# Performance work log

Hardware: AMD Instinct MI355X
Metric: run time of the kernel (lower is better)

## Reference

```python
import jax, jax.numpy as jnp
import numpy as np

B, D_CAT, C_IN, C_OUT, K, H, W = 16, 512, 256, 256, 3, 64, 64


def setup_inputs() -> dict:
    key = jax.random.key(0)
    ks = jax.random.split(key, 9)
    inp = {
        "x": jax.random.normal(ks[0], (B, C_IN, H, W), dtype=jnp.float32),
        "y": jax.random.normal(ks[1], (B, D_CAT), dtype=jnp.float32),
        # EqualLinear stack: d_catin -> in_channels, then n_dl=2 layers in_channels -> in_channels
        "w0": jax.random.normal(ks[2], (C_IN, D_CAT), dtype=jnp.float32) / np.sqrt(D_CAT),
        "b0": jnp.zeros((C_IN,), dtype=jnp.float32),
        "w1": jax.random.normal(ks[3], (C_IN, C_IN), dtype=jnp.float32) / np.sqrt(C_IN),
        "b1": jnp.zeros((C_IN,), dtype=jnp.float32),
        "w2": jax.random.normal(ks[4], (C_IN, C_IN), dtype=jnp.float32) / np.sqrt(C_IN),
        "b2": jnp.zeros((C_IN,), dtype=jnp.float32),
        # shared conv weight (O, I, k, k), modulated per sample
        "conv_w": jax.random.normal(ks[5], (C_OUT, C_IN, K, K), dtype=jnp.float32) / np.sqrt(C_IN * K * K),
    }
    return inp


def _lrelu(z):
    # nn.LeakyReLU default negative_slope = 0.01
    return jnp.where(z >= 0, z, 0.01 * z)


def reference(x, y, w0, b0, w1, b1, w2, b2, conv_w):
    # style MLP (EqualLinear stack with LeakyReLU)
    s = _lrelu(y @ w0.T + b0)          # (B, C_in)
    s = _lrelu(s @ w1.T + b1)
    s = _lrelu(s @ w2.T + b2)
    # Per-sample weight modulation: conv(x[b], W * s[b, None, :, None, None]).
    # Since the scale is per input channel (no demodulation), this is exactly
    # equivalent to scaling the input channels and running one shared conv —
    # the fused form a custom kernel would use.
    x_mod = x * s[:, :, None, None]    # (B, C_in, H, W)
    out = jax.lax.conv_general_dilated(
        x_mod, conv_w,
        window_strides=(1, 1),
        padding=((1, 1), (1, 1)),
        dimension_numbers=("NCHW", "OIHW", "NCHW"),
    )  # (B, C_out, H, W); conv has bias=False in _DyConv
    return out
```

## Files before the change

kernel.cpp:

```cpp
#include <hip/hip_runtime.h>

typedef short bf16x8 __attribute__((ext_vector_type(8)));
typedef float f32x4 __attribute__((ext_vector_type(4)));
typedef unsigned short ushort8 __attribute__((ext_vector_type(8)));
typedef unsigned short ushort4v __attribute__((ext_vector_type(4)));

#define BATCH 16
#define DCAT 512
#define CIN 256
#define COUT 256
#define HH 64
#define WW 64
#define HP 66
#define WP 66
#define PLANE (HP * WP * 8)
#define AHALO 52224
#define BBUF 32768

__device__ __forceinline__ unsigned short f2bf(float f) {
  unsigned int u = __float_as_uint(f);
  unsigned int r = (u + 0x7fffu + ((u >> 16) & 1u)) >> 16;
  return (unsigned short)r;
}

template <int IN_DIM>
__global__ void __launch_bounds__(256) mlp_layer(const float* __restrict__ in,
                                                 const float* __restrict__ w,
                                                 const float* __restrict__ bias,
                                                 float* __restrict__ out) {
  int wid = threadIdx.x >> 6, lane = threadIdx.x & 63;
  int oidx = blockIdx.x * 4 + wid;
  int b = oidx >> 8, c = oidx & 255;
  const float* wr = w + (size_t)c * IN_DIM;
  const float* ir = in + (size_t)b * IN_DIM;
  float sum = 0.f;
#pragma unroll
  for (int d0 = 0; d0 < IN_DIM; d0 += 256) {
    f32x4 wv = *(const f32x4*)(wr + d0 + lane * 4);
    f32x4 iv = *(const f32x4*)(ir + d0 + lane * 4);
    sum += wv[0] * iv[0] + wv[1] * iv[1] + wv[2] * iv[2] + wv[3] * iv[3];
  }
#pragma unroll
  for (int off = 32; off; off >>= 1) sum += __shfl_xor(sum, off, 64);
  if (lane == 0) {
    float a = sum + bias[c];
    out[oidx] = a >= 0.f ? a : 0.01f * a;
  }
}

__global__ void __launch_bounds__(256) prep_all(const float* __restrict__ t1,
                                                const float* __restrict__ w2,
                                                const float* __restrict__ b2,
                                                const float* __restrict__ x,
                                                const float* __restrict__ cw,
                                                unsigned short* __restrict__ xpad,
                                                unsigned short* __restrict__ wt) {
  int blk = blockIdx.x;
  int tid = threadIdx.x;

  if (blk >= 1024) {
    int idx = (blk - 1024) * 256 + tid;
    int t = idx / 16384;
    int r = idx - t * 16384;
    int o = r >> 6, i4 = r & 63;
    ushort4v v;
#pragma unroll
    for (int j = 0; j < 4; j++) v[j] = f2bf(cw[(o * 256 + i4 * 4 + j) * 9 + t]);
    *(ushort4v*)(wt + ((size_t)(t * COUT + o)) * CIN + i4 * 4) = v;
    return;
  }

  int h = blk & 1, c8 = (blk >> 1) & 31, b = blk >> 6;
  int wid = tid >> 6, lane = tid & 63;

  float tv = t1[b * CIN + tid];
  float pj[8];
#pragma unroll
  for (int j = 0; j < 8; j++) pj[j] = w2[(size_t)(c8 * 8 + j) * CIN + tid] * tv;

  const float* xb = x + ((size_t)(b * CIN + c8 * 8)) * (HH * WW);
  int gg0 = h * 512 + tid;
  int gg1 = gg0 + 256;
  int hh0 = (gg0 >> 4) + 1, w00 = (gg0 & 15) * 4 + 1;
  int hh1 = (gg1 >> 4) + 1, w01 = (gg1 & 15) * 4 + 1;
  int base0 = (hh0 - 1) * WW + (w00 - 1);
  int base1 = (hh1 - 1) * WW + (w01 - 1);
  f32x4 v0[8], v1[8];
#pragma unroll
  for (int j = 0; j < 8; j++) v0[j] = *(const f32x4*)(xb + j * (HH * WW) + base0);
#pragma unroll
  for (int j = 0; j < 8; j++) v1[j] = *(const f32x4*)(xb + j * (HH * WW) + base1);

#pragma unroll
  for (int off = 32; off; off >>= 1)
#pragma unroll
    for (int j = 0; j < 8; j++) pj[j] += __shfl_xor(pj[j], off, 64);
  __shared__ float red[4][8];
  __shared__ float sv_sh[8];
  if (lane == 0)
#pragma unroll
    for (int j = 0; j < 8; j++) red[wid][j] = pj[j];
  __syncthreads();
  if (tid < 8) {
    float a = red[0][tid] + red[1][tid] + red[2][tid] + red[3][tid] + b2[c8 * 8 + tid];
    sv_sh[tid] = a >= 0.f ? a : 0.01f * a;
  }
  __syncthreads();
  float sv[8];
#pragma unroll
  for (int j = 0; j < 8; j++) sv[j] = sv_sh[j];

  unsigned short* xp = xpad + ((size_t)(b * 32 + c8)) * PLANE;

  if (tid < 130) {
    int i = h * 130 + tid;
    int bh, bw;
    if (i < 66) { bh = 0; bw = i; }
    else if (i < 132) { bh = 65; bw = i - 66; }
    else if (i < 196) { bh = i - 132 + 1; bw = 0; }
    else { bh = i - 196 + 1; bw = 65; }
    ushort8 z = {0, 0, 0, 0, 0, 0, 0, 0};
    *(ushort8*)(xp + (bh * WP + bw) * 8) = z;
  }

  unsigned short* op0 = xp + (hh0 * WP + w00) * 8;
  unsigned short* op1 = xp + (hh1 * WP + w01) * 8;
#pragma unroll
  for (int t2 = 0; t2 < 4; t2++) {
    ushort8 o;
#pragma unroll
    for (int j = 0; j < 8; j++) o[j] = f2bf(v0[j][t2] * sv[j]);
    *(ushort8*)(op0 + t2 * 8) = o;
  }
#pragma unroll
  for (int t2 = 0; t2 < 4; t2++) {
    ushort8 o;
#pragma unroll
    for (int j = 0; j < 8; j++) o[j] = f2bf(v1[j][t2] * sv[j]);
    *(ushort8*)(op1 + t2 * 8) = o;
  }
}

__device__ __forceinline__ void gl2lds16(const void* g, void* l) {
  __builtin_amdgcn_global_load_lds((const __attribute__((address_space(1))) void*)g,
                                   (__attribute__((address_space(3))) void*)l, 16, 0, 0);
}

__global__ void __launch_bounds__(512, 1) gemm_conv(const unsigned short* __restrict__ xpad,
                                                    const unsigned short* __restrict__ wt,
                                                    float* __restrict__ out) {
  __shared__ __align__(16) char lds[AHALO + 2 * BBUF];
  int tid = threadIdx.x;
  int wid = tid >> 6, lane = tid & 63;
  int bid = blockIdx.x;
  int m_t = (bid & 7) * 32 + (bid >> 3);
  int m0 = m_t << 8;
  int b = m0 >> 12;
  int h0 = (m0 >> 6) & 63;
  int wm = wid & 1, wn = wid >> 1;

  f32x4 acc[8][4];
#pragma unroll
  for (int mi = 0; mi < 8; mi++)
#pragma unroll
    for (int ni = 0; ni < 4; ni++) acc[mi][ni] = (f32x4){0.f, 0.f, 0.f, 0.f};

  const unsigned short* aSrc[7];
#pragma unroll
  for (int i = 0; i < 7; i++) {
    int c = (i * 8 + wid) * 64 + lane;
    int e = c >> 3, cs = c & 7;
    int gs = cs ^ (e & 7);
    int rh = e / 68, wc = e - rh * 68;
    aSrc[i] = xpad + ((size_t)((b * 32 + gs) * HP + (h0 + rh))) * (WP * 8) + wc * 8;
  }

  int o_l = tid >> 3;
  int csb = tid & 7;
  const unsigned short* bL = wt + o_l * CIN + ((csb ^ (o_l & 7)) * 8);

  int qa = lane >> 4;
  int l15 = lane & 15;
  int rB = wn * 64 + l15;
  int offB0 = rB * 128 + ((qa ^ (rB & 7)) * 16);
  int offB1 = rB * 128 + (((qa + 4) ^ (rB & 7)) * 16);

  int cur = 0;
  for (int kc2 = 0; kc2 < 4; kc2++) {
    size_t kofs = (size_t)kc2 * 8 * PLANE;
#pragma unroll
    for (int i = 0; i < 6; i++)
      gl2lds16(aSrc[i] + kofs, lds + (i * 8 + wid) * 1024);
    if (wid < 3) gl2lds16(aSrc[6] + kofs, lds + (48 + wid) * 1024);
    if (kc2 == 0) {
      const unsigned short* bG = bL;
      char* dB = lds + AHALO + wid * 1024;
#pragma unroll
      for (int q = 0; q < 4; q++) gl2lds16(bG + q * 64 * CIN, dB + q * 8192);
    }
    __syncthreads();

    for (int kh = 0; kh < 3; kh++) {
      for (int kw = 0; kw < 3; kw++) {
        int tap = kh * 3 + kw;
        if (tap < 8 || kc2 < 3) {
          const unsigned short* bG = (tap < 8)
              ? bL + (tap + 1) * (COUT * CIN) + kc2 * 64
              : bL + (kc2 + 1) * 64;
          char* dB = lds + AHALO + (cur ^ 1) * BBUF + wid * 1024;
#pragma unroll
          for (int q = 0; q < 4; q++) gl2lds16(bG + q * 64 * CIN, dB + q * 8192);
        }

        int eb = (wm * 2 + kh) * 68 + l15 + kw;
        int s0 = eb & 7, s1 = (eb + 4) & 7;
        int a00 = eb * 128 + ((qa ^ s0) * 16);
        int a01 = (eb + 68) * 128 + ((qa ^ s1) * 16);
        int a10 = eb * 128 + (((qa + 4) ^ s0) * 16);
        int a11 = (eb + 68) * 128 + (((qa + 4) ^ s1) * 16);
        const char* Bb = lds + AHALO + cur * BBUF;

        bf16x8 av[8], bv0[4], aw[8], bv1[4];
#pragma unroll
        for (int mi = 0; mi < 4; mi++) {
          av[mi] = *(const bf16x8*)(lds + a00 + mi * 2048);
          av[4 + mi] = *(const bf16x8*)(lds + a01 + mi * 2048);
        }
#pragma unroll
        for (int ni = 0; ni < 4; ni++)
          bv0[ni] = *(const bf16x8*)(Bb + offB0 + ni * 2048);

#pragma unroll
        for (int mi = 0; mi < 4; mi++) {
          aw[mi] = *(const bf16x8*)(lds + a10 + mi * 2048);
          aw[4 + mi] = *(const bf16x8*)(lds + a11 + mi * 2048);
        }
#pragma unroll
        for (int ni = 0; ni < 4; ni++)
          bv1[ni] = *(const bf16x8*)(Bb + offB1 + ni * 2048);

        __builtin_amdgcn_s_setprio(1);
#pragma unroll
        for (int mi = 0; mi < 8; mi++)
#pragma unroll
          for (int ni = 0; ni < 4; ni++)
            acc[mi][ni] = __builtin_amdgcn_mfma_f32_16x16x32_bf16(av[mi], bv0[ni],
                                                                  acc[mi][ni], 0, 0, 0);
#pragma unroll
        for (int mi = 0; mi < 8; mi++)
#pragma unroll
          for (int ni = 0; ni < 4; ni++)
            acc[mi][ni] = __builtin_amdgcn_mfma_f32_16x16x32_bf16(aw[mi], bv1[ni],
                                                                  acc[mi][ni], 0, 0, 0);
        __builtin_amdgcn_s_setprio(0);

        __syncthreads();
        cur ^= 1;
      }
    }
  }

  int pixbase = m0 & 4095;
  int quad = lane >> 4;
  int col = lane & 15;
#pragma unroll
  for (int mi = 0; mi < 8; mi++) {
    int pm = pixbase + wm * 128 + mi * 16 + quad * 4;
#pragma unroll
    for (int ni = 0; ni < 4; ni++) {
      int on = wn * 64 + ni * 16 + col;
      float* op = out + ((size_t)(b * COUT + on) << 12) + pm;
      *(f32x4*)op = acc[mi][ni];
    }
  }
}

extern "C" void kernel_launch(void* const* d_in, const int* in_sizes, int n_in,
                              void* d_out, int out_size, void* d_ws, size_t ws_size,
                              hipStream_t stream) {
  const float* x = (const float*)d_in[0];
  const float* y = (const float*)d_in[1];
  const float* w0 = (const float*)d_in[2];
  const float* b0 = (const float*)d_in[3];
  const float* w1 = (const float*)d_in[4];
  const float* b1 = (const float*)d_in[5];
  const float* w2 = (const float*)d_in[6];
  const float* b2 = (const float*)d_in[7];
  const float* cw = (const float*)d_in[8];
  float* out = (float*)d_out;

  char* ws = (char*)d_ws;
  unsigned short* xpad = (unsigned short*)ws;
  unsigned short* wt = (unsigned short*)(ws + 35684352);
  float* t0 = (float*)(ws + 35684352 + 2359296);
  float* t1 = (float*)(ws + 35684352 + 2359296 + 16384);

  mlp_layer<DCAT><<<BATCH * CIN / 4, 256, 0, stream>>>(y, w0, b0, t0);
  mlp_layer<CIN><<<BATCH * CIN / 4, 256, 0, stream>>>(t0, w1, b1, t1);
  prep_all<<<1024 + 576, 256, 0, stream>>>(t1, w2, b2, x, cw, xpad, wt);
  gemm_conv<<<BATCH * HH * WW / 256, 512, 0, stream>>>(xpad, wt, out);
}
```

Measured before the change: 241.1 us.

## Halve conv GEMM block to 4 waves, each computing a 128x128 tile

The implicit-GEMM conv kernel drops from 8 waves of 512 threads to 4 waves of 256 threads. Each wave now owns a 128x128 output sub-tile (8x8 MFMA accumulators) instead of 128x64, which doubles register reuse of the A fragments per LDS read. The A-halo and B staging loops are rewritten so fewer threads issue twice as many global-to-LDS loads. It cuts LDS read traffic per MFMA but raises register pressure (256 accumulator floats per lane) and halves the waves available to hide latency.

```diff
diff --git a/kernel.cpp b/kernel.cpp
--- a/kernel.cpp
+++ b/kernel.cpp
@@ -146,7 +146,7 @@
                                    (__attribute__((address_space(3))) void*)l, 16, 0, 0);
 }
 
-__global__ void __launch_bounds__(512, 1) gemm_conv(const unsigned short* __restrict__ xpad,
+__global__ void __launch_bounds__(256, 1) gemm_conv(const unsigned short* __restrict__ xpad,
                                                     const unsigned short* __restrict__ wt,
                                                     float* __restrict__ out) {
   __shared__ __align__(16) char lds[AHALO + 2 * BBUF];
@@ -159,45 +159,48 @@
   int h0 = (m0 >> 6) & 63;
   int wm = wid & 1, wn = wid >> 1;
 
-  f32x4 acc[8][4];
+  f32x4 acc[8][8];
 #pragma unroll
   for (int mi = 0; mi < 8; mi++)
 #pragma unroll
-    for (int ni = 0; ni < 4; ni++) acc[mi][ni] = (f32x4){0.f, 0.f, 0.f, 0.f};
-
-  const unsigned short* aSrc[7];
-#pragma unroll
-  for (int i = 0; i < 7; i++) {
-    int c = (i * 8 + wid) * 64 + lane;
-    int e = c >> 3, cs = c & 7;
-    int gs = cs ^ (e & 7);
-    int rh = e / 68, wc = e - rh * 68;
-    aSrc[i] = xpad + ((size_t)((b * 32 + gs) * HP + (h0 + rh))) * (WP * 8) + wc * 8;
-  }
+    for (int ni = 0; ni < 8; ni++) acc[mi][ni] = (f32x4){0.f, 0.f, 0.f, 0.f};
 
   int o_l = tid >> 3;
   int csb = tid & 7;
   const unsigned short* bL = wt + o_l * CIN + ((csb ^ (o_l & 7)) * 8);
 
+#define STAGE_B(BUF, BG)                                                \
+  do {                                                                  \
+    char* dB = lds + AHALO + (BUF) * BBUF + wid * 1024;                 \
+    _Pragma("unroll")                                                   \
+    for (int q = 0; q < 4; q++) {                                       \
+      gl2lds16((BG) + q * 64 * CIN, dB + q * 8192);                     \
+      gl2lds16((BG) + q * 64 * CIN + 32 * CIN, dB + q * 8192 + 4096);   \
+    }                                                                   \
+  } while (0)
+
   int qa = lane >> 4;
   int l15 = lane & 15;
-  int rB = wn * 64 + l15;
-  int offB0 = rB * 128 + ((qa ^ (rB & 7)) * 16);
-  int offB1 = rB * 128 + (((qa + 4) ^ (rB & 7)) * 16);
+  int offB0 = (wn * 128 + l15) * 128 + ((qa ^ (l15 & 7)) * 16);
+  int offB1 = (wn * 128 + l15) * 128 + (((qa + 4) ^ (l15 & 7)) * 16);
 
   int cur = 0;
   for (int kc2 = 0; kc2 < 4; kc2++) {
     size_t kofs = (size_t)kc2 * 8 * PLANE;
 #pragma unroll
-    for (int i = 0; i < 6; i++)
-      gl2lds16(aSrc[i] + kofs, lds + (i * 8 + wid) * 1024);
-    if (wid < 3) gl2lds16(aSrc[6] + kofs, lds + (48 + wid) * 1024);
-    if (kc2 == 0) {
-      const unsigned short* bG = bL;
-      char* dB = lds + AHALO + wid * 1024;
-#pragma unroll
-      for (int q = 0; q < 4; q++) gl2lds16(bG + q * 64 * CIN, dB + q * 8192);
+    for (int i = 0; i < 13; i++) {
+      int g = i * 4 + wid;
+      if (i < 12 || wid < 3) {
+        int e = g * 8 + (lane >> 3);
+        int gs = csb ^ (e & 7);
+        int rh = e / 68;
+        int wc = e - rh * 68;
+        const unsigned short* src =
+            xpad + ((size_t)((b * 32 + gs) * HP + (h0 + rh))) * (WP * 8) + wc * 8 + kofs;
+        gl2lds16(src, lds + g * 1024);
+      }
     }
+    if (kc2 == 0) STAGE_B(0, bL);
     __syncthreads();
 
     for (int kh = 0; kh < 3; kh++) {
@@ -207,9 +210,7 @@
           const unsigned short* bG = (tap < 8)
               ? bL + (tap + 1) * (COUT * CIN) + kc2 * 64
               : bL + (kc2 + 1) * 64;
-          char* dB = lds + AHALO + (cur ^ 1) * BBUF + wid * 1024;
-#pragma unroll
-          for (int q = 0; q < 4; q++) gl2lds16(bG + q * 64 * CIN, dB + q * 8192);
+          STAGE_B(cur ^ 1, bG);
         }
 
         int eb = (wm * 2 + kh) * 68 + l15 + kw;
@@ -220,36 +221,35 @@
         int a11 = (eb + 68) * 128 + (((qa + 4) ^ s1) * 16);
         const char* Bb = lds + AHALO + cur * BBUF;
 
-        bf16x8 av[8], bv0[4], aw[8], bv1[4];
+        bf16x8 av[8], bv0[8], aw[8], bv1[8];
 #pragma unroll
         for (int mi = 0; mi < 4; mi++) {
           av[mi] = *(const bf16x8*)(lds + a00 + mi * 2048);
           av[4 + mi] = *(const bf16x8*)(lds + a01 + mi * 2048);
         }
 #pragma unroll
-        for (int ni = 0; ni < 4; ni++)
+        for (int ni = 0; ni < 8; ni++)
           bv0[ni] = *(const bf16x8*)(Bb + offB0 + ni * 2048);
-
 #pragma unroll
         for (int mi = 0; mi < 4; mi++) {
           aw[mi] = *(const bf16x8*)(lds + a10 + mi * 2048);
           aw[4 + mi] = *(const bf16x8*)(lds + a11 + mi * 2048);
         }
 #pragma unroll
-        for (int ni = 0; ni < 4; ni++)
+        for (int ni = 0; ni < 8; ni++)
           bv1[ni] = *(const bf16x8*)(Bb + offB1 + ni * 2048);
 
         __builtin_amdgcn_s_setprio(1);
 #pragma unroll
         for (int mi = 0; mi < 8; mi++)
 #pragma unroll
-          for (int ni = 0; ni < 4; ni++)
+          for (int ni = 0; ni < 8; ni++)
             acc[mi][ni] = __builtin_amdgcn_mfma_f32_16x16x32_bf16(av[mi], bv0[ni],
                                                                   acc[mi][ni], 0, 0, 0);
 #pragma unroll
         for (int mi = 0; mi < 8; mi++)
 #pragma unroll
-          for (int ni = 0; ni < 4; ni++)
+          for (int ni = 0; ni < 8; ni++)
             acc[mi][ni] = __builtin_amdgcn_mfma_f32_16x16x32_bf16(aw[mi], bv1[ni],
                                                                   acc[mi][ni], 0, 0, 0);
         __builtin_amdgcn_s_setprio(0);
@@ -267,8 +267,8 @@
   for (int mi = 0; mi < 8; mi++) {
     int pm = pixbase + wm * 128 + mi * 16 + quad * 4;
 #pragma unroll
-    for (int ni = 0; ni < 4; ni++) {
-      int on = wn * 64 + ni * 16 + col;
+    for (int ni = 0; ni < 8; ni++) {
+      int on = wn * 128 + ni * 16 + col;
       float* op = out + ((size_t)(b * COUT + on) << 12) + pm;
       *(f32x4*)op = acc[mi][ni];
     }
@@ -298,5 +298,5 @@
   mlp_layer<DCAT><<<BATCH * CIN / 4, 256, 0, stream>>>(y, w0, b0, t0);
   mlp_layer<CIN><<<BATCH * CIN / 4, 256, 0, stream>>>(t0, w1, b1, t1);
   prep_all<<<1024 + 576, 256, 0, stream>>>(t1, w2, b2, x, cw, xpad, wt);
-  gemm_conv<<<BATCH * HH * WW / 256, 512, 0, stream>>>(xpad, wt, out);
-}
+  gemm_conv<<<BATCH * HH * WW / 256, 256, 0, stream>>>(xpad, wt, out);
+}
```

Measured after the change: 272.6 us. 13.1% more time.

## Replace full syncthreads with counted vmcnt waits and split-phase MFMA barriers

Applied to the files above, without the earlier changes.

Each tap's work is split into two K-half phases. Each phase loads its A and B fragments from LDS, then waits with raw s_barrier and explicit s_waitcnt instead of __syncthreads. The vmcnt(4) wait lets the next tap's B prefetch stay in flight while the current tile is consumed, rather than draining all global loads at every barrier. A staging moves to the end of each channel chunk, after all reads of the current halo. This adds more barriers per tap, and correctness now depends on exact outstanding-load counts.

```diff
diff --git a/kernel.cpp b/kernel.cpp
--- a/kernel.cpp
+++ b/kernel.cpp
@@ -145,6 +145,10 @@
   __builtin_amdgcn_global_load_lds((const __attribute__((address_space(1))) void*)g,
                                    (__attribute__((address_space(3))) void*)l, 16, 0, 0);
 }
+
+#define WAIT_LGKM0()                                        \
+  asm volatile("s_waitcnt lgkmcnt(0)" ::: "memory");        \
+  __builtin_amdgcn_sched_barrier(0)
 
 __global__ void __launch_bounds__(512, 1) gemm_conv(const unsigned short* __restrict__ xpad,
                                                     const unsigned short* __restrict__ wt,
@@ -185,32 +189,33 @@
   int offB0 = rB * 128 + ((qa ^ (rB & 7)) * 16);
   int offB1 = rB * 128 + (((qa + 4) ^ (rB & 7)) * 16);
 
+#define STAGE_B4(BUF, BG)                                               \
+  do {                                                                  \
+    char* dB_ = lds + AHALO + (BUF) * BBUF + wid * 1024;                \
+    const unsigned short* bg_ = (BG);                                   \
+    _Pragma("unroll")                                                   \
+    for (int q = 0; q < 4; q++) gl2lds16(bg_ + q * 64 * CIN, dB_ + q * 8192); \
+  } while (0)
+
+#define STAGE_A(KOFS)                                                   \
+  do {                                                                  \
+    size_t ko_ = (KOFS);                                                \
+    _Pragma("unroll")                                                   \
+    for (int i = 0; i < 6; i++)                                         \
+      gl2lds16(aSrc[i] + ko_, lds + (i * 8 + wid) * 1024);              \
+    if (wid < 3) gl2lds16(aSrc[6] + ko_, lds + (48 + wid) * 1024);      \
+  } while (0)
+
+  STAGE_A(0);
+  STAGE_B4(0, bL);
+  asm volatile("s_waitcnt vmcnt(0)" ::: "memory");
+  __builtin_amdgcn_s_barrier();
+
   int cur = 0;
   for (int kc2 = 0; kc2 < 4; kc2++) {
-    size_t kofs = (size_t)kc2 * 8 * PLANE;
-#pragma unroll
-    for (int i = 0; i < 6; i++)
-      gl2lds16(aSrc[i] + kofs, lds + (i * 8 + wid) * 1024);
-    if (wid < 3) gl2lds16(aSrc[6] + kofs, lds + (48 + wid) * 1024);
-    if (kc2 == 0) {
-      const unsigned short* bG = bL;
-      char* dB = lds + AHALO + wid * 1024;
-#pragma unroll
-      for (int q = 0; q < 4; q++) gl2lds16(bG + q * 64 * CIN, dB + q * 8192);
-    }
-    __syncthreads();
-
     for (int kh = 0; kh < 3; kh++) {
       for (int kw = 0; kw < 3; kw++) {
         int tap = kh * 3 + kw;
-        if (tap < 8 || kc2 < 3) {
-          const unsigned short* bG = (tap < 8)
-              ? bL + (tap + 1) * (COUT * CIN) + kc2 * 64
-              : bL + (kc2 + 1) * 64;
-          char* dB = lds + AHALO + (cur ^ 1) * BBUF + wid * 1024;
-#pragma unroll
-          for (int q = 0; q < 4; q++) gl2lds16(bG + q * 64 * CIN, dB + q * 8192);
-        }
 
         int eb = (wm * 2 + kh) * 68 + l15 + kw;
         int s0 = eb & 7, s1 = (eb + 4) & 7;
@@ -220,43 +225,65 @@
         int a11 = (eb + 68) * 128 + (((qa + 4) ^ s1) * 16);
         const char* Bb = lds + AHALO + cur * BBUF;
 
-        bf16x8 av[8], bv0[4], aw[8], bv1[4];
-#pragma unroll
-        for (int mi = 0; mi < 4; mi++) {
-          av[mi] = *(const bf16x8*)(lds + a00 + mi * 2048);
-          av[4 + mi] = *(const bf16x8*)(lds + a01 + mi * 2048);
+        if (tap < 8) {
+          STAGE_B4(cur ^ 1, bL + (size_t)(tap + 1) * (COUT * CIN) + kc2 * 64);
+        } else if (kc2 < 3) {
+          STAGE_B4(cur ^ 1, bL + (kc2 + 1) * 64);
         }
-#pragma unroll
-        for (int ni = 0; ni < 4; ni++)
-          bv0[ni] = *(const bf16x8*)(Bb + offB0 + ni * 2048);
-
-#pragma unroll
-        for (int mi = 0; mi < 4; mi++) {
-          aw[mi] = *(const bf16x8*)(lds + a10 + mi * 2048);
-          aw[4 + mi] = *(const bf16x8*)(lds + a11 + mi * 2048);
+        {
+          bf16x8 av[8], bv[4];
+#pragma unroll
+          for (int mi = 0; mi < 4; mi++) {
+            av[mi] = *(const bf16x8*)(lds + a00 + mi * 2048);
+            av[4 + mi] = *(const bf16x8*)(lds + a01 + mi * 2048);
+          }
+#pragma unroll
+          for (int ni = 0; ni < 4; ni++)
+            bv[ni] = *(const bf16x8*)(Bb + offB0 + ni * 2048);
+          asm volatile("s_waitcnt vmcnt(4)" ::: "memory");
+          __builtin_amdgcn_s_barrier();
+          WAIT_LGKM0();
+          __builtin_amdgcn_s_setprio(1);
+#pragma unroll
+          for (int mi = 0; mi < 8; mi++)
+#pragma unroll
+            for (int ni = 0; ni < 4; ni++)
+              acc[mi][ni] = __builtin_amdgcn_mfma_f32_16x16x32_bf16(av[mi], bv[ni],
+                                                                    acc[mi][ni], 0, 0, 0);
+          __builtin_amdgcn_s_setprio(0);
+          __builtin_amdgcn_s_barrier();
         }
-#pragma unroll
-        for (int ni = 0; ni < 4; ni++)
-          bv1[ni] = *(const bf16x8*)(Bb + offB1 + ni * 2048);
-
-        __builtin_amdgcn_s_setprio(1);
-#pragma unroll
-        for (int mi = 0; mi < 8; mi++)
+
+        {
+          bf16x8 aw[8], bw[4];
+#pragma unroll
+          for (int mi = 0; mi < 4; mi++) {
+            aw[mi] = *(const bf16x8*)(lds + a10 + mi * 2048);
+            aw[4 + mi] = *(const bf16x8*)(lds + a11 + mi * 2048);
+          }
 #pragma unroll
           for (int ni = 0; ni < 4; ni++)
-            acc[mi][ni] = __builtin_amdgcn_mfma_f32_16x16x32_bf16(av[mi], bv0[ni],
-                                                                  acc[mi][ni], 0, 0, 0);
-#pragma unroll
-        for (int mi = 0; mi < 8; mi++)
-#pragma unroll
-          for (int ni = 0; ni < 4; ni++)
-            acc[mi][ni] = __builtin_amdgcn_mfma_f32_16x16x32_bf16(aw[mi], bv1[ni],
-                                                                  acc[mi][ni], 0, 0, 0);
-        __builtin_amdgcn_s_setprio(0);
-
-        __syncthreads();
+            bw[ni] = *(const bf16x8*)(Bb + offB1 + ni * 2048);
+          __builtin_amdgcn_s_barrier();
+          WAIT_LGKM0();
+          __builtin_amdgcn_s_setprio(1);
+#pragma unroll
+          for (int mi = 0; mi < 8; mi++)
+#pragma unroll
+            for (int ni = 0; ni < 4; ni++)
+              acc[mi][ni] = __builtin_amdgcn_mfma_f32_16x16x32_bf16(aw[mi], bw[ni],
+                                                                    acc[mi][ni], 0, 0, 0);
+          __builtin_amdgcn_s_setprio(0);
+          __builtin_amdgcn_s_barrier();
+        }
+
         cur ^= 1;
       }
+    }
+    if (kc2 < 3) {
+      STAGE_A((size_t)(kc2 + 1) * 8 * PLANE);
+      asm volatile("s_waitcnt vmcnt(0)" ::: "memory");
+      __builtin_amdgcn_s_barrier();
     }
   }
 
```

Result: faster. 228.3 us (-5.3%).
